# Performance work log

Measured on AMD Instinct MI355X. Metric: run time of the kernel, lower is better.

The kernel has to match this reference:

```python
import jax, jax.numpy as jnp
import numpy as np

E, T = 8, 256          # n_experts, chunk length
IN, OUT = 1024, 1024   # input_size, output_size
D1, D2 = 32, 32        # nearest factors of IN
DO1, DO2 = 32, 32      # nearest factors of OUT
B, L = 8, 2048
LOSS_COEF = 1e-5


def setup_inputs() -> dict:
    key = jax.random.key(0)
    ks = jax.random.split(key, 12)
    eyeE = lambda d, k: (jnp.broadcast_to(jnp.eye(d, dtype=jnp.float32), (E, d, d))
                         + 0.01 * jax.random.normal(k, (E, d, d), jnp.float32))
    return {
        "x": jax.random.normal(ks[0], (B, L, IN), jnp.float32),
        "w_gate": 0.02 * jax.random.normal(ks[1], (IN, E), jnp.float32),
        "weight": 0.02 * jax.random.normal(ks[2], (E, OUT, IN), jnp.float32),
        "bias": 0.02 * jax.random.normal(ks[3], (E, OUT), jnp.float32),
        "res_weight": 0.02 * jax.random.normal(ks[4], (OUT, IN), jnp.float32),
        "res_bias": 0.02 * jax.random.normal(ks[5], (1, OUT), jnp.float32),
        "curve1_in": eyeE(D1, ks[6]),
        "curve2_in": eyeE(D2, ks[7]),
        "curve1_out": eyeE(DO1, ks[8]),
        "curve2_out": eyeE(DO2, ks[9]),
        "curve1_bias": eyeE(DO1, ks[10]),
        "curve2_bias": eyeE(DO2, ks[11]),
    }


def _cv_squared(v):
    v = v.astype(jnp.float32)
    return jnp.var(v, ddof=1) / (jnp.mean(v) ** 2 + 1e-10)


def reference(x, w_gate, weight, bias, res_weight, res_bias,
              curve1_in, curve2_in, curve1_out, curve2_out,
              curve1_bias, curve2_bias):
    Bx, Lx, d = x.shape
    N = Lx // T
    BN = Bx * N
    xr = x.reshape(BN, T, d)

    # --- gating (eval mode, ties_merging forces k = n_experts -> plain softmax) ---
    logits = xr.mean(axis=1) @ w_gate            # [BN, E]
    gates = jax.nn.softmax(logits, axis=1)        # [BN, E]
    load = (gates > 0).sum(axis=0).astype(jnp.float32)
    importance = gates.sum(axis=0)
    loss = (_cv_squared(importance) + _cv_squared(load)) * LOSS_COEF

    # --- roll gates by one segment, keeping each sample's first chunk (detached) ---
    e_first = jax.lax.stop_gradient(gates.reshape(Bx, N, E)[:, 0])
    g = jnp.roll(gates, 1, axis=0).reshape(Bx, N, E)
    g = g.at[:, 0].set(e_first).reshape(BN, E)

    # --- Kronecker curve-factored expert weight merge ---
    rw = (weight - res_weight).reshape(E, DO1, DO2, D1, D2)
    rw = jnp.einsum('bij,bjklm->biklm', curve1_out, rw)
    rw = jnp.einsum('bik,bjklm->bjilm', curve2_out, rw)
    rw = jnp.einsum('bil,bjklm->bjkim', curve1_in, rw)
    rw = jnp.einsum('bim,bjklm->bjkli', curve2_in, rw)
    rw = rw.reshape(E, OUT, IN)
    expert_weights = res_weight + jnp.einsum('be,eoi->boi', g, rw)  # [BN, O, I]

    y = jnp.einsum('bij,bkj->bik', xr, expert_weights)  # [BN, T, O]

    # --- curve-factored expert bias merge ---
    rb = (bias - res_bias).reshape(E, DO1, DO2)
    rb = jnp.einsum('bki,bij->bkj', curve1_bias, rb)      # [E, DO1, DO2]
    rb = jnp.einsum('bkj,bij->bik', curve2_bias, rb)      # [E, DO1, DO2]
    rb = rb.reshape(E, OUT)
    expert_bias = res_bias + jnp.einsum('be,eo->bo', g, rb)  # [BN, O]

    y = (y + expert_bias[:, None, :]).reshape(Bx, Lx, OUT)
    return y, loss
```

## Files before the change

kernel.cpp:

```cpp
#include <hip/hip_runtime.h>
#include <cstdint>

typedef __bf16 bf16x8 __attribute__((ext_vector_type(8)));
typedef float  f32x4  __attribute__((ext_vector_type(4)));
using u16 = unsigned short;

struct alignas(8) u16x4 { u16 x, y, z, w; };

__device__ __forceinline__ u16 f2bf(float f) {
  unsigned u = __builtin_bit_cast(unsigned, f);
  u = (u + 0x7FFFu + ((u >> 16) & 1u)) >> 16;
  return (u16)u;
}
__device__ __forceinline__ float bf2f(u16 u) {
  unsigned v = ((unsigned)u) << 16;
  return __builtin_bit_cast(float, v);
}

#define ASYNC16(gp, lp) __builtin_amdgcn_global_load_lds( \
    (__attribute__((address_space(1))) void*)(void*)(gp),  \
    (__attribute__((address_space(3))) void*)(lp), 16, 0, 0)

static constexpr size_t OFF_XBF  = 0;
static constexpr size_t OFF_EW   = 33554432;
static constexpr size_t OFF_T2   = 33554432;
static constexpr size_t OFF_PM   = 67108864;
static constexpr size_t OFF_RW   = 167772160;
static constexpr size_t OFF_LG   = 201326592;
static constexpr size_t OFF_G    = 201588736;
static constexpr size_t OFF_RB   = 201592832;
static constexpr size_t OFF_EB   = 201625600;
static constexpr size_t WS_NEED  = 201887744;

__global__ __launch_bounds__(256) void k_means(const float* __restrict__ x,
                                               float* __restrict__ pm,
                                               u16* __restrict__ xbf) {
  int b = blockIdx.x, q = blockIdx.y, tid = threadIdx.x;
  const float* xb = x + (size_t)b * 262144 + (size_t)q * 16384;
  u16* xo = xbf + (size_t)b * 262144 + (size_t)q * 16384;
  float s0 = 0.f, s1 = 0.f, s2 = 0.f, s3 = 0.f;
  for (int t = 0; t < 16; ++t) {
    const float* row = xb + t * 1024;
    u16* orow = xo + t * 1024;
    float v0 = row[tid], v1 = row[tid + 256], v2 = row[tid + 512], v3 = row[tid + 768];
    s0 += v0; s1 += v1; s2 += v2; s3 += v3;
    orow[tid] = f2bf(v0); orow[tid + 256] = f2bf(v1);
    orow[tid + 512] = f2bf(v2); orow[tid + 768] = f2bf(v3);
  }
  float* p = pm + ((size_t)b * 16 + q) * 1024;
  p[tid] = s0; p[tid + 256] = s1; p[tid + 512] = s2; p[tid + 768] = s3;
}

__global__ __launch_bounds__(256) void k_redlogits(const float* __restrict__ pm,
                                                   const float* __restrict__ w_gate,
                                                   float* __restrict__ logits) {
  __shared__ float red[4][8];
  int b = blockIdx.x, tid = threadIdx.x;
  const float* p = pm + (size_t)b * 16384 + tid * 4;
  float4 s = {0.f, 0.f, 0.f, 0.f};
#pragma unroll
  for (int q = 0; q < 16; ++q) {
    float4 v = *(const float4*)(p + q * 1024);
    s.x += v.x; s.y += v.y; s.z += v.z; s.w += v.w;
  }
  int i0 = tid * 4;
  float acc[8];
#pragma unroll
  for (int e = 0; e < 8; ++e) {
    acc[e] = s.x * w_gate[(i0 + 0) * 8 + e] + s.y * w_gate[(i0 + 1) * 8 + e]
           + s.z * w_gate[(i0 + 2) * 8 + e] + s.w * w_gate[(i0 + 3) * 8 + e];
  }
#pragma unroll
  for (int off = 32; off >= 1; off >>= 1)
#pragma unroll
    for (int e = 0; e < 8; ++e) acc[e] += __shfl_down(acc[e], off, 64);
  int wv = tid >> 6;
  if ((tid & 63) == 0)
#pragma unroll
    for (int e = 0; e < 8; ++e) red[wv][e] = acc[e];
  __syncthreads();
  if (tid < 8)
    logits[b * 8 + tid] =
        (red[0][tid] + red[1][tid] + red[2][tid] + red[3][tid]) * (1.f / 256.f);
}

__global__ __launch_bounds__(64) void k_gatefin(const float* __restrict__ logits,
                                                float* __restrict__ g,
                                                float* __restrict__ loss_out) {
  __shared__ float gates[64][8];
  __shared__ float imp[8];
  int b = threadIdx.x;
  {
    float lg[8];
#pragma unroll
    for (int j = 0; j < 8; ++j) lg[j] = logits[b * 8 + j];
    float mx = lg[0];
#pragma unroll
    for (int j = 1; j < 8; ++j) mx = fmaxf(mx, lg[j]);
    float s = 0.f, ex[8];
#pragma unroll
    for (int j = 0; j < 8; ++j) { ex[j] = expf(lg[j] - mx); s += ex[j]; }
    float inv = 1.f / s;
#pragma unroll
    for (int j = 0; j < 8; ++j) gates[b][j] = ex[j] * inv;
  }
  __syncthreads();
  if (b < 8) {
    float s = 0.f;
    for (int bb = 0; bb < 64; ++bb) s += gates[bb][b];
    imp[b] = s;
  }
  __syncthreads();
  if (b == 0) {
    float mean = 0.f;
#pragma unroll
    for (int j = 0; j < 8; ++j) mean += imp[j];
    mean *= (1.f / 8.f);
    float var = 0.f;
#pragma unroll
    for (int j = 0; j < 8; ++j) { float d = imp[j] - mean; var += d * d; }
    var *= (1.f / 7.f);
    loss_out[0] = (var / (mean * mean + 1e-10f)) * 1e-5f;
  }
  __syncthreads();
  {
    int src = ((b & 7) == 0) ? b : b - 1;
#pragma unroll
    for (int j = 0; j < 8; ++j) g[b * 8 + j] = gates[src][j];
  }
}

__global__ __launch_bounds__(256) void k_mergeA(const float* __restrict__ W,
                                                const float* __restrict__ R,
                                                const float* __restrict__ c1o,
                                                const float* __restrict__ c2o,
                                                float* __restrict__ T2t) {
  __shared__ float dw[8 * 1024];
  __shared__ float m1[1024], m2[1024];
  int e = blockIdx.y, c0 = blockIdx.x * 8, tid = threadIdx.x;
  const float* We = W + (size_t)e * 1048576;
  for (int idx = tid; idx < 1024; idx += 256) {
    m1[idx] = c1o[e * 1024 + idx];
    m2[idx] = c2o[e * 1024 + idx];
  }
  {
    int r = tid >> 1, h = (tid & 1) * 4;
#pragma unroll
    for (int i = 0; i < 8; ++i) {
      int row = r + i * 128;
      const float4 wv = *(const float4*)(We + (size_t)row * 1024 + c0 + h);
      const float4 rv = *(const float4*)(R + (size_t)row * 1024 + c0 + h);
      dw[(h + 0) * 1024 + row] = wv.x - rv.x;
      dw[(h + 1) * 1024 + row] = wv.y - rv.y;
      dw[(h + 2) * 1024 + row] = wv.z - rv.z;
      dw[(h + 3) * 1024 + row] = wv.w - rv.w;
    }
  }
  __syncthreads();
  int i1 = tid & 31, c = tid >> 5;
  const float* dwc = dw + c * 1024;
  float U[32];
#pragma unroll
  for (int k = 0; k < 32; ++k) U[k] = 0.f;
  for (int j = 0; j < 32; ++j) {
    float cj = m1[i1 * 32 + j];
    const float4* rowp = (const float4*)(dwc + j * 32);
#pragma unroll
    for (int k4 = 0; k4 < 8; ++k4) {
      float4 v = rowp[k4];
      U[k4 * 4 + 0] += cj * v.x; U[k4 * 4 + 1] += cj * v.y;
      U[k4 * 4 + 2] += cj * v.z; U[k4 * 4 + 3] += cj * v.w;
    }
  }
  float* obase = T2t + (size_t)e * 1048576 + (size_t)(c0 + c) * 1024 + i1 * 32;
#pragma unroll
  for (int g4 = 0; g4 < 8; ++g4) {
    float s[4];
#pragma unroll
    for (int q = 0; q < 4; ++q) {
      const float4* m2r = (const float4*)(m2 + (g4 * 4 + q) * 32);
      float acc = 0.f;
#pragma unroll
      for (int k4 = 0; k4 < 8; ++k4) {
        float4 mv = m2r[k4];
        acc += mv.x * U[k4 * 4 + 0] + mv.y * U[k4 * 4 + 1]
             + mv.z * U[k4 * 4 + 2] + mv.w * U[k4 * 4 + 3];
      }
      s[q] = acc;
    }
    float4 o4; o4.x = s[0]; o4.y = s[1]; o4.z = s[2]; o4.w = s[3];
    *(float4*)(obase + g4 * 4) = o4;
  }
}

__global__ __launch_bounds__(256) void k_mergeB(const float* __restrict__ T2t,
                                                const float* __restrict__ c1i,
                                                const float* __restrict__ c2i,
                                                u16* __restrict__ RWbf) {
  __shared__ float t2[8 * 1024];
  __shared__ float m1[1024], m2[1024];
  int e = blockIdx.y, o0 = blockIdx.x * 8, tid = threadIdx.x;
  const float* Te = T2t + (size_t)e * 1048576;
  for (int idx = tid; idx < 1024; idx += 256) {
    m1[idx] = c1i[e * 1024 + idx];
    m2[idx] = c2i[e * 1024 + idx];
  }
  {
    int r = tid >> 1, h = (tid & 1) * 4;
#pragma unroll
    for (int i = 0; i < 8; ++i) {
      int row = r + i * 128;
      const float4 tv = *(const float4*)(Te + (size_t)row * 1024 + o0 + h);
      t2[(h + 0) * 1024 + row] = tv.x;
      t2[(h + 1) * 1024 + row] = tv.y;
      t2[(h + 2) * 1024 + row] = tv.z;
      t2[(h + 3) * 1024 + row] = tv.w;
    }
  }
  __syncthreads();
  int i1 = tid & 31, oc = tid >> 5;
  const float* t2c = t2 + oc * 1024;
  float A[32];
#pragma unroll
  for (int m = 0; m < 32; ++m) A[m] = 0.f;
  for (int l = 0; l < 32; ++l) {
    float cl = m1[i1 * 32 + l];
    const float4* rowp = (const float4*)(t2c + l * 32);
#pragma unroll
    for (int m4 = 0; m4 < 8; ++m4) {
      float4 v = rowp[m4];
      A[m4 * 4 + 0] += cl * v.x; A[m4 * 4 + 1] += cl * v.y;
      A[m4 * 4 + 2] += cl * v.z; A[m4 * 4 + 3] += cl * v.w;
    }
  }
  u16* obase = RWbf + ((size_t)e * 1024 + o0 + oc) * 1024 + i1 * 32;
#pragma unroll
  for (int g4 = 0; g4 < 8; ++g4) {
    float s[4];
#pragma unroll
    for (int q = 0; q < 4; ++q) {
      const float4* m2r = (const float4*)(m2 + (g4 * 4 + q) * 32);
      float acc = 0.f;
#pragma unroll
      for (int m4 = 0; m4 < 8; ++m4) {
        float4 mv = m2r[m4];
        acc += mv.x * A[m4 * 4 + 0] + mv.y * A[m4 * 4 + 1]
             + mv.z * A[m4 * 4 + 2] + mv.w * A[m4 * 4 + 3];
      }
      s[q] = acc;
    }
    u16x4 o4; o4.x = f2bf(s[0]); o4.y = f2bf(s[1]); o4.z = f2bf(s[2]); o4.w = f2bf(s[3]);
    *(u16x4*)(obase + g4 * 4) = o4;
  }
}

__global__ __launch_bounds__(256) void k_rb(const float* __restrict__ bias,
                                            const float* __restrict__ res_bias,
                                            const float* __restrict__ c1b,
                                            const float* __restrict__ c2b,
                                            float* __restrict__ rb) {
  __shared__ float rb0[32][33], rb1[32][33], m1[32][32], m2[32][32];
  int e = blockIdx.x, tid = threadIdx.x;
  for (int idx = tid; idx < 1024; idx += 256) {
    int i = idx >> 5, j = idx & 31;
    rb0[i][j] = bias[e * 1024 + idx] - res_bias[idx];
    m1[i][j] = c1b[e * 1024 + idx];
    m2[i][j] = c2b[e * 1024 + idx];
  }
  __syncthreads();
  for (int idx = tid; idx < 1024; idx += 256) {
    int p = idx >> 5, j = idx & 31;
    float s = 0.f;
#pragma unroll
    for (int i = 0; i < 32; ++i) s += m1[p][i] * rb0[i][j];
    rb1[p][j] = s;
  }
  __syncthreads();
  for (int idx = tid; idx < 1024; idx += 256) {
    int p = idx >> 5, q = idx & 31;
    float s = 0.f;
#pragma unroll
    for (int j = 0; j < 32; ++j) s += m2[q][j] * rb1[p][j];
    rb[e * 1024 + idx] = s;
  }
}

__global__ __launch_bounds__(256) void k_eb(const float* __restrict__ rb,
                                            const float* __restrict__ res_bias,
                                            const float* __restrict__ g,
                                            float* __restrict__ eb) {
  int b = blockIdx.x, tid = threadIdx.x;
  for (int o = tid; o < 1024; o += 256) {
    float a = res_bias[o];
#pragma unroll
    for (int e = 0; e < 8; ++e) a += g[b * 8 + e] * rb[e * 1024 + o];
    eb[b * 1024 + o] = a;
  }
}

__global__ __launch_bounds__(256) void k_combine(const u16* __restrict__ RWbf,
                                                 const float* __restrict__ R,
                                                 const float* __restrict__ g,
                                                 u16* __restrict__ EW) {
  __shared__ float gs[512];
  int o = blockIdx.x, tid = threadIdx.x;
  for (int idx = tid; idx < 512; idx += 256) gs[idx] = g[idx];
  __syncthreads();
  int i0 = tid * 4;
  float4 r4 = *(const float4*)(R + (size_t)o * 1024 + i0);
  float4 w[8];
#pragma unroll
  for (int e = 0; e < 8; ++e) {
    u16x4 t = *(const u16x4*)(RWbf + (size_t)e * 1048576 + (size_t)o * 1024 + i0);
    w[e].x = bf2f(t.x); w[e].y = bf2f(t.y); w[e].z = bf2f(t.z); w[e].w = bf2f(t.w);
  }
  for (int b = 0; b < 64; ++b) {
    float a0 = r4.x, a1 = r4.y, a2 = r4.z, a3 = r4.w;
#pragma unroll
    for (int e = 0; e < 8; ++e) {
      float ge = gs[b * 8 + e];
      a0 += ge * w[e].x; a1 += ge * w[e].y; a2 += ge * w[e].z; a3 += ge * w[e].w;
    }
    u16x4 u; u.x = f2bf(a0); u.y = f2bf(a1); u.z = f2bf(a2); u.w = f2bf(a3);
    *(u16x4*)(EW + (size_t)b * 1048576 + (size_t)o * 1024 + i0) = u;
  }
}

__global__ __launch_bounds__(512) void k_gemm(const u16* __restrict__ Xb,
                                              const u16* __restrict__ EW,
                                              const float* __restrict__ eb,
                                              float* __restrict__ Y) {
  __shared__ alignas(16) u16 As[2][256 * 64];
  __shared__ alignas(16) u16 Bs[2][256 * 64];
  int hw = blockIdx.x;
  int b  = (hw & 7) * 8 + (hw >> 5);
  int nt = (hw >> 3) & 3;
  int t0 = b * 256, o0 = nt * 256;
  int tid = threadIdx.x, lane = tid & 63, wv = tid >> 6;
  int wr = wv >> 2, wc = wv & 3;
  f32x4 acc[8][4] = {};
  const u16* aG = Xb + (size_t)t0 * 1024;
  const u16* bG = EW + (size_t)b * 1048576 + (size_t)o0 * 1024;
  int srow = tid >> 3;
  int scol = (tid & 7) << 3;
  int gcol = (((tid & 7) ^ (srow & 7)) << 3);
  int lr = lane & 15;
  int sx = lr & 7;
#pragma unroll
  for (int iss = 0; iss < 4; ++iss) {
    int r = srow + iss * 64;
    ASYNC16(aG + (size_t)r * 1024 + gcol, &As[0][r * 64 + scol]);
    ASYNC16(bG + (size_t)r * 1024 + gcol, &Bs[0][r * 64 + scol]);
  }
  __syncthreads();
  for (int kt = 0; kt < 16; ++kt) {
    int cur = kt & 1;
    if (kt < 15) {
      int k0 = (kt + 1) << 6;
#pragma unroll
      for (int iss = 0; iss < 4; ++iss) {
        int r = srow + iss * 64;
        ASYNC16(aG + (size_t)r * 1024 + k0 + gcol, &As[cur ^ 1][r * 64 + scol]);
        ASYNC16(bG + (size_t)r * 1024 + k0 + gcol, &Bs[cur ^ 1][r * 64 + scol]);
      }
    }
#pragma unroll
    for (int kk = 0; kk < 2; ++kk) {
      int c16 = kk * 4 + (lane >> 4);
      int cp = ((c16 ^ sx) << 3);
      bf16x8 af[8], bfr[4];
#pragma unroll
      for (int mi = 0; mi < 8; ++mi)
        af[mi] = *(const bf16x8*)&As[cur][(wr * 128 + mi * 16 + lr) * 64 + cp];
#pragma unroll
      for (int ni = 0; ni < 4; ++ni)
        bfr[ni] = *(const bf16x8*)&Bs[cur][(wc * 64 + ni * 16 + lr) * 64 + cp];
#pragma unroll
      for (int mi = 0; mi < 8; ++mi)
#pragma unroll
        for (int ni = 0; ni < 4; ++ni)
          acc[mi][ni] = __builtin_amdgcn_mfma_f32_16x16x32_bf16(af[mi], bfr[ni], acc[mi][ni], 0, 0, 0);
    }
    __syncthreads();
  }
  int rbase = (lane >> 4) << 2;
#pragma unroll
  for (int ni = 0; ni < 4; ++ni) {
    int o = o0 + wc * 64 + ni * 16 + lr;
    float ebv = eb[b * 1024 + o];
#pragma unroll
    for (int mi = 0; mi < 8; ++mi) {
      int trow = t0 + wr * 128 + mi * 16 + rbase;
      float* yp = Y + (size_t)trow * 1024 + o;
      yp[0]    = acc[mi][ni][0] + ebv;
      yp[1024] = acc[mi][ni][1] + ebv;
      yp[2048] = acc[mi][ni][2] + ebv;
      yp[3072] = acc[mi][ni][3] + ebv;
    }
  }
}

extern "C" void kernel_launch(void* const* d_in, const int* in_sizes, int n_in,
                              void* d_out, int out_size, void* d_ws, size_t ws_size,
                              hipStream_t stream) {
  const float* x      = (const float*)d_in[0];
  const float* w_gate = (const float*)d_in[1];
  const float* weight = (const float*)d_in[2];
  const float* bias   = (const float*)d_in[3];
  const float* res_w  = (const float*)d_in[4];
  const float* res_b  = (const float*)d_in[5];
  const float* c1i    = (const float*)d_in[6];
  const float* c2i    = (const float*)d_in[7];
  const float* c1o    = (const float*)d_in[8];
  const float* c2o    = (const float*)d_in[9];
  const float* c1b    = (const float*)d_in[10];
  const float* c2b    = (const float*)d_in[11];
  float* y = (float*)d_out;

  if (ws_size < WS_NEED) return;

  char* wsb = (char*)d_ws;
  u16*   xbf   = (u16*)(wsb + OFF_XBF);
  u16*   EW    = (u16*)(wsb + OFF_EW);
  float* T2t   = (float*)(wsb + OFF_T2);
  float* pm    = (float*)(wsb + OFF_PM);
  u16*   RWbf  = (u16*)(wsb + OFF_RW);
  float* lgts  = (float*)(wsb + OFF_LG);
  float* g     = (float*)(wsb + OFF_G);
  float* rb    = (float*)(wsb + OFF_RB);
  float* eb    = (float*)(wsb + OFF_EB);

  k_means    <<<dim3(64, 16), 256, 0, stream>>>(x, pm, xbf);
  k_redlogits<<<64, 256, 0, stream>>>(pm, w_gate, lgts);
  k_gatefin  <<<1, 64, 0, stream>>>(lgts, g, y + 16777216);
  k_mergeA   <<<dim3(128, 8), 256, 0, stream>>>(weight, res_w, c1o, c2o, T2t);
  k_mergeB   <<<dim3(128, 8), 256, 0, stream>>>(T2t, c1i, c2i, RWbf);
  k_rb       <<<8, 256, 0, stream>>>(bias, res_b, c1b, c2b, rb);
  k_eb       <<<64, 256, 0, stream>>>(rb, res_b, g, eb);
  k_combine  <<<1024, 256, 0, stream>>>(RWbf, res_w, g, EW);
  k_gemm     <<<256, 512, 0, stream>>>(xbf, EW, eb, y);
}
```

Before: 243.4 us.

## Single-buffer GEMM LDS for higher occupancy and vectorize mean kernel

The GEMM kernel drops the double-buffered LDS tiles in favour of a single buffer. Each k-step now loads its tile and then synchronises, and launch_bounds asks for 4 blocks per CU. This halves LDS use so more blocks can be resident, at the cost of losing the prefetch overlap within a block. The mean/convert kernel is also switched to float4 loads and packed bf16 stores with an unrolled loop.

```diff
diff --git a/kernel.cpp b/kernel.cpp
--- a/kernel.cpp
+++ b/kernel.cpp
@@ -36,19 +36,18 @@
                                                float* __restrict__ pm,
                                                u16* __restrict__ xbf) {
   int b = blockIdx.x, q = blockIdx.y, tid = threadIdx.x;
-  const float* xb = x + (size_t)b * 262144 + (size_t)q * 16384;
-  u16* xo = xbf + (size_t)b * 262144 + (size_t)q * 16384;
+  const float* xb = x + (size_t)b * 262144 + (size_t)q * 16384 + tid * 4;
+  u16* xo = xbf + (size_t)b * 262144 + (size_t)q * 16384 + tid * 4;
   float s0 = 0.f, s1 = 0.f, s2 = 0.f, s3 = 0.f;
+#pragma unroll
   for (int t = 0; t < 16; ++t) {
-    const float* row = xb + t * 1024;
-    u16* orow = xo + t * 1024;
-    float v0 = row[tid], v1 = row[tid + 256], v2 = row[tid + 512], v3 = row[tid + 768];
-    s0 += v0; s1 += v1; s2 += v2; s3 += v3;
-    orow[tid] = f2bf(v0); orow[tid + 256] = f2bf(v1);
-    orow[tid + 512] = f2bf(v2); orow[tid + 768] = f2bf(v3);
-  }
-  float* p = pm + ((size_t)b * 16 + q) * 1024;
-  p[tid] = s0; p[tid + 256] = s1; p[tid + 512] = s2; p[tid + 768] = s3;
+    float4 v = *(const float4*)(xb + t * 1024);
+    s0 += v.x; s1 += v.y; s2 += v.z; s3 += v.w;
+    u16x4 o; o.x = f2bf(v.x); o.y = f2bf(v.y); o.z = f2bf(v.z); o.w = f2bf(v.w);
+    *(u16x4*)(xo + t * 1024) = o;
+  }
+  float4 sv; sv.x = s0; sv.y = s1; sv.z = s2; sv.w = s3;
+  *(float4*)(pm + ((size_t)b * 16 + q) * 1024 + tid * 4) = sv;
 }
 
 __global__ __launch_bounds__(256) void k_redlogits(const float* __restrict__ pm,
@@ -326,14 +325,15 @@
   }
 }
 
-__global__ __launch_bounds__(512) void k_gemm(const u16* __restrict__ Xb,
-                                              const u16* __restrict__ EW,
-                                              const float* __restrict__ eb,
-                                              float* __restrict__ Y) {
-  __shared__ alignas(16) u16 As[2][256 * 64];
-  __shared__ alignas(16) u16 Bs[2][256 * 64];
+__global__ __launch_bounds__(512, 4) void k_gemm(const u16* __restrict__ Xb,
+                                                 const u16* __restrict__ EW,
+                                                 const float* __restrict__ eb,
+                                                 float* __restrict__ Y) {
+  __shared__ alignas(16) u16 As[256 * 64];
+  __shared__ alignas(16) u16 Bs[256 * 64];
   int hw = blockIdx.x;
-  int b  = (hw & 7) * 8 + (hw >> 5);
+  int xcd = hw & 7;
+  int b  = xcd * 8 + (hw >> 5);
   int nt = (hw >> 3) & 3;
   int t0 = b * 256, o0 = nt * 256;
   int tid = threadIdx.x, lane = tid & 63, wv = tid >> 6;
@@ -346,24 +346,15 @@
   int gcol = (((tid & 7) ^ (srow & 7)) << 3);
   int lr = lane & 15;
   int sx = lr & 7;
-#pragma unroll
-  for (int iss = 0; iss < 4; ++iss) {
-    int r = srow + iss * 64;
-    ASYNC16(aG + (size_t)r * 1024 + gcol, &As[0][r * 64 + scol]);
-    ASYNC16(bG + (size_t)r * 1024 + gcol, &Bs[0][r * 64 + scol]);
-  }
-  __syncthreads();
   for (int kt = 0; kt < 16; ++kt) {
-    int cur = kt & 1;
-    if (kt < 15) {
-      int k0 = (kt + 1) << 6;
-#pragma unroll
-      for (int iss = 0; iss < 4; ++iss) {
-        int r = srow + iss * 64;
-        ASYNC16(aG + (size_t)r * 1024 + k0 + gcol, &As[cur ^ 1][r * 64 + scol]);
-        ASYNC16(bG + (size_t)r * 1024 + k0 + gcol, &Bs[cur ^ 1][r * 64 + scol]);
-      }
-    }
+    int k0 = kt << 6;
+#pragma unroll
+    for (int iss = 0; iss < 4; ++iss) {
+      int r = srow + iss * 64;
+      ASYNC16(aG + (size_t)r * 1024 + k0 + gcol, &As[r * 64 + scol]);
+      ASYNC16(bG + (size_t)r * 1024 + k0 + gcol, &Bs[r * 64 + scol]);
+    }
+    __syncthreads();
 #pragma unroll
     for (int kk = 0; kk < 2; ++kk) {
       int c16 = kk * 4 + (lane >> 4);
@@ -371,10 +362,10 @@
       bf16x8 af[8], bfr[4];
 #pragma unroll
       for (int mi = 0; mi < 8; ++mi)
-        af[mi] = *(const bf16x8*)&As[cur][(wr * 128 + mi * 16 + lr) * 64 + cp];
+        af[mi] = *(const bf16x8*)&As[(wr * 128 + mi * 16 + lr) * 64 + cp];
 #pragma unroll
       for (int ni = 0; ni < 4; ++ni)
-        bfr[ni] = *(const bf16x8*)&Bs[cur][(wc * 64 + ni * 16 + lr) * 64 + cp];
+        bfr[ni] = *(const bf16x8*)&Bs[(wc * 64 + ni * 16 + lr) * 64 + cp];
 #pragma unroll
       for (int mi = 0; mi < 8; ++mi)
 #pragma unroll
```

Result: slower. 398.1 us (+63.6%).
